# Optimization experiments

Hardware: AMD Instinct MI355X
Metric: run time of the kernel (lower is better)

The kernel has to match this reference:

```python
import jax, jax.numpy as jnp
import numpy as np

EMBED = 1024
HEADS = 16
HEAD_DIM = EMBED // HEADS
B, N = 2, 2048


def setup_inputs() -> dict:
    key = jax.random.key(0)
    ks = jax.random.split(key, 7)
    s = 1.0 / np.sqrt(EMBED)
    x = jax.random.normal(ks[0], (B, N, EMBED), dtype=jnp.float32)
    # causal mask: 1 where attention allowed, 0 elsewhere (masked_fill on mask==0)
    mask = jnp.tril(jnp.ones((N, N), dtype=jnp.int32))[None, None, :, :]
    Wq = jax.random.uniform(ks[1], (EMBED, EMBED), jnp.float32, -s, s)
    Wk = jax.random.uniform(ks[2], (EMBED, EMBED), jnp.float32, -s, s)
    Wv = jax.random.uniform(ks[3], (EMBED, EMBED), jnp.float32, -s, s)
    Wo = jax.random.uniform(ks[4], (EMBED, EMBED), jnp.float32, -s, s)
    bo = jax.random.uniform(ks[5], (EMBED,), jnp.float32, -s, s)
    return {"x": x, "mask": mask, "Wq": Wq, "Wk": Wk, "Wv": Wv, "Wo": Wo, "bo": bo}


def reference(x, mask, Wq, Wk, Wv, Wo, bo):
    Bx, Nx, D = x.shape
    # torch nn.Linear: y = x @ W.T
    q = (x @ Wq.T).reshape(Bx, Nx, HEADS, HEAD_DIM).transpose(0, 2, 1, 3)
    k = (x @ Wk.T).reshape(Bx, Nx, HEADS, HEAD_DIM).transpose(0, 2, 1, 3)
    v = (x @ Wv.T).reshape(Bx, Nx, HEADS, HEAD_DIM).transpose(0, 2, 1, 3)
    score = jnp.einsum('bhqd,bhkd->bhqk', q, k) / np.sqrt(HEAD_DIM).astype(np.float32)
    score = jnp.where(mask == 0, -jnp.inf, score)
    probs = jax.nn.softmax(score, axis=-1)
    out = jnp.einsum('bhqk,bhkd->bhqd', probs, v)  # [B,H,N,hd]
    out = out.transpose(0, 2, 1, 3).reshape(Bx, Nx, D)
    return out @ Wo.T + bo
```

## Files before the change

### kernel.cpp

```cpp
#include <hip/hip_runtime.h>
#include <hip/hip_bf16.h>

#define B_  2
#define N_  2048
#define E_  1024
#define H_  16
#define HD_ 64
#define M_  (B_*N_)
#define RSZ ((size_t)M_ * E_)

typedef short bf16x8 __attribute__((ext_vector_type(8)));
typedef float f32x4 __attribute__((ext_vector_type(4)));
typedef unsigned short u16x8 __attribute__((ext_vector_type(8)));

#define AS1 __attribute__((address_space(1)))
#define AS3 __attribute__((address_space(3)))

__device__ __forceinline__ unsigned short f2bfu(float f) {
    __hip_bfloat16 h = __float2bfloat16(f);
    return *reinterpret_cast<unsigned short*>(&h);
}
__device__ __forceinline__ unsigned int pack2bf(float lo, float hi) {
    return ((unsigned int)f2bfu(hi) << 16) | (unsigned int)f2bfu(lo);
}
#define MFMA16(a,b,c) __builtin_amdgcn_mfma_f32_16x16x32_bf16((a),(b),(c),0,0,0)

__device__ __forceinline__ void gl_lds16(const void* g, void* l) {
    __builtin_amdgcn_global_load_lds((const AS1 void*)g, (AS3 void*)l, 16, 0, 0);
}

__global__ __launch_bounds__(256) void fconv_all_kernel(
    const float* __restrict__ x,
    const float* __restrict__ Wq, const float* __restrict__ Wk,
    const float* __restrict__ Wv, const float* __restrict__ Wo,
    unsigned short* __restrict__ xbf, unsigned short* __restrict__ wbf)
{
    const int bid = blockIdx.x;
    const float* src;
    unsigned short* dst;
    int off;
    if (bid < 2048) {
        src = x; dst = xbf; off = bid * 2048 + threadIdx.x * 8;
    } else {
        const int z = (bid - 2048) >> 9;
        src = (z == 0) ? Wq : (z == 1 ? Wk : (z == 2 ? Wv : Wo));
        dst = wbf + (size_t)z * E_ * E_;
        off = ((bid - 2048) & 511) * 2048 + threadIdx.x * 8;
    }
    const float4 a = *reinterpret_cast<const float4*>(src + off);
    const float4 b = *reinterpret_cast<const float4*>(src + off + 4);
    u16x8 v;
    v[0]=f2bfu(a.x); v[1]=f2bfu(a.y); v[2]=f2bfu(a.z); v[3]=f2bfu(a.w);
    v[4]=f2bfu(b.x); v[5]=f2bfu(b.y); v[6]=f2bfu(b.z); v[7]=f2bfu(b.w);
    *reinterpret_cast<u16x8*>(dst + off) = v;
}

__global__ __launch_bounds__(256) void fconv_kernel(
    const float* __restrict__ src, unsigned short* __restrict__ dst)
{
    const int i0 = (blockIdx.x * 256 + threadIdx.x) * 8;
    const float4 a = *reinterpret_cast<const float4*>(src + i0);
    const float4 b = *reinterpret_cast<const float4*>(src + i0 + 4);
    u16x8 v;
    v[0]=f2bfu(a.x); v[1]=f2bfu(a.y); v[2]=f2bfu(a.z); v[3]=f2bfu(a.w);
    v[4]=f2bfu(b.x); v[5]=f2bfu(b.y); v[6]=f2bfu(b.z); v[7]=f2bfu(b.w);
    *reinterpret_cast<u16x8*>(dst + i0) = v;
}

__global__ __launch_bounds__(256) void qkv_glds_kernel(
    const unsigned short* __restrict__ xbf, const unsigned short* __restrict__ wbf,
    unsigned short* __restrict__ qkv)
{
    const int z = blockIdx.z;
    const unsigned short* __restrict__ W = wbf + (size_t)z * E_ * E_;
    unsigned short* __restrict__ out = qkv + (size_t)z * RSZ;
    const int m0 = blockIdx.x * 64;
    const int n0 = blockIdx.y * 128;
    __shared__ unsigned short ldsA[64*64];
    __shared__ unsigned short ldsB[128*64];
    const int t = threadIdx.x;
    const int lane = t & 63;
    const int w = t >> 6, wr = w >> 1, wc = w & 1;
    const int fr = lane & 15, fq = lane >> 4;
    const int subrow = lane >> 3;
    const int csw = ((lane & 7) ^ subrow) * 8;
    const int rcol = ((fq * 8) ^ ((fr & 7) * 8));
    f32x4 acc[2][4] = {};

    for (int kt = 0; kt < 16; ++kt) {
        const int k0 = kt * 64;
        __syncthreads();
        #pragma unroll
        for (int i = 0; i < 6; ++i) {
            const int c = w * 6 + i;
            if (c < 8) {
                const int row = c * 8 + subrow;
                gl_lds16(xbf + (size_t)(m0 + row) * E_ + k0 + csw, &ldsA[c * 512]);
            } else {
                const int row = (c - 8) * 8 + subrow;
                gl_lds16(W + (size_t)(n0 + row) * E_ + k0 + csw, &ldsB[(c - 8) * 512]);
            }
        }
        __syncthreads();
        #pragma unroll
        for (int ks = 0; ks < 2; ++ks) {
            bf16x8 af[2], bfv[4];
            #pragma unroll
            for (int mf = 0; mf < 2; ++mf)
                af[mf] = *(const bf16x8*)&ldsA[(wr*32 + mf*16 + fr)*64 + (rcol ^ (ks*32))];
            #pragma unroll
            for (int nf = 0; nf < 4; ++nf)
                bfv[nf] = *(const bf16x8*)&ldsB[(wc*64 + nf*16 + fr)*64 + (rcol ^ (ks*32))];
            #pragma unroll
            for (int mf = 0; mf < 2; ++mf)
                #pragma unroll
                for (int nf = 0; nf < 4; ++nf)
                    acc[mf][nf] = MFMA16(af[mf], bfv[nf], acc[mf][nf]);
        }
    }

    const float scale = (z == 0) ? 0.125f : 1.0f;
    #pragma unroll
    for (int mf = 0; mf < 2; ++mf) {
        #pragma unroll
        for (int r = 0; r < 4; ++r) {
            const int m = m0 + wr*32 + mf*16 + fq*4 + r;
            const int b = m >> 11, npos = m & (N_ - 1);
            #pragma unroll
            for (int nf = 0; nf < 4; ++nf) {
                const int n = n0 + wc*64 + nf*16 + fr;
                const int h = n >> 6, d = n & 63;
                const unsigned short val = f2bfu(acc[mf][nf][r] * scale);
                if (z == 2)
                    out[(((size_t)(b*H_ + h))*HD_ + d)*N_ + npos] = val;
                else
                    out[(((size_t)(b*H_ + h))*N_ + npos)*HD_ + d] = val;
            }
        }
    }
}

__global__ __launch_bounds__(256) void qkv_f32_kernel(
    const float* __restrict__ x, const unsigned short* __restrict__ wbf,
    unsigned short* __restrict__ qkv)
{
    const int z = blockIdx.z;
    const unsigned short* __restrict__ W = wbf + (size_t)z * E_ * E_;
    unsigned short* __restrict__ out = qkv + (size_t)z * RSZ;
    const int m0 = blockIdx.x * 128;
    const int n0 = blockIdx.y * 128;
    __shared__ unsigned short As[128][72];
    __shared__ unsigned short Bs[128][72];
    const int t = threadIdx.x;
    const int lane = t & 63;
    const int w = t >> 6, wr = w >> 1, wc = w & 1;
    const int fr = lane & 15, fq = lane >> 4;
    const int srow = t >> 1, scol = (t & 1) * 32;
    f32x4 acc[4][4] = {};

    const float* arow = x + (size_t)(m0 + srow) * E_ + scol;
    const unsigned short* brow = W + (size_t)(n0 + srow) * E_ + scol;

    float4 a4[8];
    u16x8 b8[4];
    #pragma unroll
    for (int i = 0; i < 8; ++i) a4[i] = reinterpret_cast<const float4*>(arow)[i];
    #pragma unroll
    for (int i = 0; i < 4; ++i) b8[i] = reinterpret_cast<const u16x8*>(brow)[i];

    for (int k0 = 0; k0 < E_; k0 += 64) {
        __syncthreads();
        #pragma unroll
        for (int j = 0; j < 4; ++j) {
            u16x8 va;
            va[0]=f2bfu(a4[2*j].x); va[1]=f2bfu(a4[2*j].y); va[2]=f2bfu(a4[2*j].z); va[3]=f2bfu(a4[2*j].w);
            va[4]=f2bfu(a4[2*j+1].x); va[5]=f2bfu(a4[2*j+1].y); va[6]=f2bfu(a4[2*j+1].z); va[7]=f2bfu(a4[2*j+1].w);
            *reinterpret_cast<u16x8*>(&As[srow][scol + 8*j]) = va;
            *reinterpret_cast<u16x8*>(&Bs[srow][scol + 8*j]) = b8[j];
        }
        __syncthreads();
        if (k0 + 64 < E_) {
            #pragma unroll
            for (int i = 0; i < 8; ++i)
                a4[i] = reinterpret_cast<const float4*>(arow + k0 + 64)[i];
            #pragma unroll
            for (int i = 0; i < 4; ++i)
                b8[i] = reinterpret_cast<const u16x8*>(brow + k0 + 64)[i];
        }
        #pragma unroll
        for (int ks = 0; ks < 2; ++ks) {
            bf16x8 af[4], bfv[4];
            #pragma unroll
            for (int mf = 0; mf < 4; ++mf)
                af[mf] = *reinterpret_cast<const bf16x8*>(&As[wr*64 + mf*16 + fr][ks*32 + fq*8]);
            #pragma unroll
            for (int nf = 0; nf < 4; ++nf)
                bfv[nf] = *reinterpret_cast<const bf16x8*>(&Bs[wc*64 + nf*16 + fr][ks*32 + fq*8]);
            #pragma unroll
            for (int mf = 0; mf < 4; ++mf)
                #pragma unroll
                for (int nf = 0; nf < 4; ++nf)
                    acc[mf][nf] = MFMA16(af[mf], bfv[nf], acc[mf][nf]);
        }
    }

    const float scale = (z == 0) ? 0.125f : 1.0f;
    #pragma unroll
    for (int mf = 0; mf < 4; ++mf) {
        #pragma unroll
        for (int r = 0; r < 4; ++r) {
            const int m = m0 + wr*64 + mf*16 + fq*4 + r;
            const int b = m >> 11, npos = m & (N_ - 1);
            #pragma unroll
            for (int nf = 0; nf < 4; ++nf) {
                const int n = n0 + wc*64 + nf*16 + fr;
                const int h = n >> 6, d = n & 63;
                const unsigned short val = f2bfu(acc[mf][nf][r] * scale);
                if (z == 2)
                    out[(((size_t)(b*H_ + h))*HD_ + d)*N_ + npos] = val;
                else
                    out[(((size_t)(b*H_ + h))*N_ + npos)*HD_ + d] = val;
            }
        }
    }
}

__global__ __launch_bounds__(512) void attn_mfma_kernel(
    const unsigned short* __restrict__ qkv, unsigned short* __restrict__ attn_out)
{
    const int bh = blockIdx.x;
    const int xp = blockIdx.y;
    const unsigned short* Qp  = qkv + (size_t)bh * N_ * HD_;
    const unsigned short* Kp  = qkv + RSZ + (size_t)bh * N_ * HD_;
    const unsigned short* Vtp = qkv + 2*RSZ + (size_t)bh * N_ * HD_;
    __shared__ unsigned short Ks[64][72], Vt[64][72];
    const int t = threadIdx.x;
    const int lane = t & 63, w = t >> 6;
    const int fr = lane & 15, fq = lane >> 4;
    const int srow = t >> 3, sc0 = (t & 7) * 8;
    const int qbase = (w < 4) ? ((31 - xp) * 64 + w * 16)
                              : (xp * 64 + (w - 4) * 16);
    const int KT = 32 - xp;
    const int ql = qbase + fr;
    const int lane_b0 = (2 * (fq & 1)) * 16 + fr;
    const int lane_b1 = lane_b0 + 16;
    const bool hi_sel = (fq >> 1) != 0;

    bf16x8 qfr[2];
    #pragma unroll
    for (int ks = 0; ks < 2; ++ks)
        qfr[ks] = *reinterpret_cast<const bf16x8*>(
            Qp + (size_t)ql * HD_ + ks*32 + fq*8);

    float m_run = -1e30f, l_run = 0.f;
    f32x4 o[4] = {};

    u16x8 kreg = *reinterpret_cast<const u16x8*>(Kp + (size_t)srow * HD_ + sc0);
    u16x8 vreg = *reinterpret_cast<const u16x8*>(Vtp + (size_t)srow * N_ + sc0);

    for (int kt = 0; kt < KT; ++kt) {
        const int k0 = kt * 64;
        __syncthreads();
        *reinterpret_cast<u16x8*>(&Ks[srow][sc0]) = kreg;
        *reinterpret_cast<u16x8*>(&Vt[srow][sc0]) = vreg;
        __syncthreads();
        if (kt + 1 < KT) {
            kreg = *reinterpret_cast<const u16x8*>(Kp + (size_t)(k0 + 64 + srow) * HD_ + sc0);
            vreg = *reinterpret_cast<const u16x8*>(Vtp + (size_t)srow * N_ + k0 + 64 + sc0);
        }
        if (k0 > qbase + 15) continue;

        f32x4 s[4] = {};
        __builtin_amdgcn_s_setprio(1);
        #pragma unroll
        for (int ks = 0; ks < 2; ++ks) {
            bf16x8 bk[4];
            #pragma unroll
            for (int nf = 0; nf < 4; ++nf)
                bk[nf] = *reinterpret_cast<const bf16x8*>(&Ks[nf*16 + fr][ks*32 + fq*8]);
            #pragma unroll
            for (int nf = 0; nf < 4; ++nf)
                s[nf] = MFMA16(bk[nf], qfr[ks], s[nf]);
        }
        __builtin_amdgcn_s_setprio(0);

        if (k0 + 63 > qbase) {
            #pragma unroll
            for (int nf = 0; nf < 4; ++nf)
                #pragma unroll
                for (int r = 0; r < 4; ++r)
                    if (k0 + nf*16 + fq*4 + r > ql) s[nf][r] = -1e30f;
        }

        float pm = -1e30f;
        #pragma unroll
        for (int nf = 0; nf < 4; ++nf)
            pm = fmaxf(pm, fmaxf(fmaxf(s[nf][0], s[nf][1]),
                                 fmaxf(s[nf][2], s[nf][3])));
        pm = fmaxf(pm, __shfl_xor(pm, 16));
        pm = fmaxf(pm, __shfl_xor(pm, 32));

        const bool need = __any(pm > m_run + 8.f);
        float scl = 1.f;
        if (need) {
            const float mnew = fmaxf(m_run, pm);
            scl = __expf(m_run - mnew);
            m_run = mnew;
        }

        float rs = 0.f;
        unsigned int u[4][2];
        #pragma unroll
        for (int nf = 0; nf < 4; ++nf) {
            const float p0 = __expf(s[nf][0] - m_run);
            const float p1 = __expf(s[nf][1] - m_run);
            const float p2 = __expf(s[nf][2] - m_run);
            const float p3 = __expf(s[nf][3] - m_run);
            rs += (p0 + p1) + (p2 + p3);
            u[nf][0] = pack2bf(p0, p1);
            u[nf][1] = pack2bf(p2, p3);
        }
        {
            float v = rs;
            v += __shfl_xor(v, 16);
            v += __shfl_xor(v, 32);
            l_run = l_run * scl + v;
        }
        if (need) {
            #pragma unroll
            for (int df = 0; df < 4; ++df)
                #pragma unroll
                for (int r = 0; r < 4; ++r)
                    o[df][r] *= scl;
        }

        bf16x8 pb[2];
        #pragma unroll
        for (int ks = 0; ks < 2; ++ks) {
            const unsigned int t00 = __shfl(u[2*ks+0][0], lane_b0);
            const unsigned int t01 = __shfl(u[2*ks+0][1], lane_b0);
            const unsigned int t02 = __shfl(u[2*ks+0][0], lane_b1);
            const unsigned int t03 = __shfl(u[2*ks+0][1], lane_b1);
            const unsigned int t10 = __shfl(u[2*ks+1][0], lane_b0);
            const unsigned int t11 = __shfl(u[2*ks+1][1], lane_b0);
            const unsigned int t12 = __shfl(u[2*ks+1][0], lane_b1);
            const unsigned int t13 = __shfl(u[2*ks+1][1], lane_b1);
            union { unsigned int wd[4]; bf16x8 v; } pu;
            pu.wd[0] = hi_sel ? t10 : t00;
            pu.wd[1] = hi_sel ? t11 : t01;
            pu.wd[2] = hi_sel ? t12 : t02;
            pu.wd[3] = hi_sel ? t13 : t03;
            pb[ks] = pu.v;
        }

        __builtin_amdgcn_s_setprio(1);
        #pragma unroll
        for (int ks = 0; ks < 2; ++ks) {
            bf16x8 bv[4];
            #pragma unroll
            for (int df = 0; df < 4; ++df)
                bv[df] = *reinterpret_cast<const bf16x8*>(&Vt[df*16 + fr][ks*32 + fq*8]);
            #pragma unroll
            for (int df = 0; df < 4; ++df)
                o[df] = MFMA16(bv[df], pb[ks], o[df]);
        }
        __builtin_amdgcn_s_setprio(0);
    }

    const int b = bh >> 4, h = bh & 15;
    const float inv = 1.0f / l_run;
    #pragma unroll
    for (int df = 0; df < 4; ++df)
        #pragma unroll
        for (int r = 0; r < 4; ++r) {
            const int d = df*16 + fq*4 + r;
            attn_out[((size_t)(b*N_ + ql))*E_ + h*64 + d] = f2bfu(o[df][r] * inv);
        }
}

__global__ __launch_bounds__(256) void out_glds_kernel(
    const unsigned short* __restrict__ A, const unsigned short* __restrict__ Wobf,
    const float* __restrict__ bo, float* __restrict__ out)
{
    const int m0 = blockIdx.x * 64;
    const int n0 = blockIdx.y * 128;
    __shared__ unsigned short ldsA[64*64];
    __shared__ unsigned short ldsB[128*64];
    const int t = threadIdx.x;
    const int lane = t & 63;
    const int w = t >> 6, wr = w >> 1, wc = w & 1;
    const int fr = lane & 15, fq = lane >> 4;
    const int subrow = lane >> 3;
    const int csw = ((lane & 7) ^ subrow) * 8;
    const int rcol = ((fq * 8) ^ ((fr & 7) * 8));
    f32x4 acc[2][4] = {};

    for (int kt = 0; kt < 16; ++kt) {
        const int k0 = kt * 64;
        __syncthreads();
        #pragma unroll
        for (int i = 0; i < 6; ++i) {
            const int c = w * 6 + i;
            if (c < 8) {
                const int row = c * 8 + subrow;
                gl_lds16(A + (size_t)(m0 + row) * E_ + k0 + csw, &ldsA[c * 512]);
            } else {
                const int row = (c - 8) * 8 + subrow;
                gl_lds16(Wobf + (size_t)(n0 + row) * E_ + k0 + csw, &ldsB[(c - 8) * 512]);
            }
        }
        __syncthreads();
        #pragma unroll
        for (int ks = 0; ks < 2; ++ks) {
            bf16x8 af[2], bfv[4];
            #pragma unroll
            for (int mf = 0; mf < 2; ++mf)
                af[mf] = *(const bf16x8*)&ldsA[(wr*32 + mf*16 + fr)*64 + (rcol ^ (ks*32))];
            #pragma unroll
            for (int nf = 0; nf < 4; ++nf)
                bfv[nf] = *(const bf16x8*)&ldsB[(wc*64 + nf*16 + fr)*64 + (rcol ^ (ks*32))];
            #pragma unroll
            for (int mf = 0; mf < 2; ++mf)
                #pragma unroll
                for (int nf = 0; nf < 4; ++nf)
                    acc[mf][nf] = MFMA16(af[mf], bfv[nf], acc[mf][nf]);
        }
    }

    #pragma unroll
    for (int mf = 0; mf < 2; ++mf) {
        #pragma unroll
        for (int r = 0; r < 4; ++r) {
            const int m = m0 + wr*32 + mf*16 + fq*4 + r;
            #pragma unroll
            for (int nf = 0; nf < 4; ++nf) {
                const int n = n0 + wc*64 + nf*16 + fr;
                out[(size_t)m * E_ + n] = acc[mf][nf][r] + bo[n];
            }
        }
    }
}

extern "C" void kernel_launch(void* const* d_in, const int* in_sizes, int n_in,
                              void* d_out, int out_size, void* d_ws, size_t ws_size,
                              hipStream_t stream) {
    const float* x  = (const float*)d_in[0];
    const float* Wq = (const float*)d_in[2];
    const float* Wk = (const float*)d_in[3];
    const float* Wv = (const float*)d_in[4];
    const float* Wo = (const float*)d_in[5];
    const float* bo = (const float*)d_in[6];
    float* out = (float*)d_out;

    unsigned short* ws = (unsigned short*)d_ws;
    const size_t need_main = 5 * RSZ * sizeof(unsigned short);

    if (ws_size >= need_main) {
        unsigned short* xbf  = ws;
        unsigned short* wbf  = ws + RSZ;
        unsigned short* qkvq = ws + 2 * RSZ;
        unsigned short* attn_ws = ws;
        unsigned short* wobf = wbf + 3 * (size_t)E_ * E_;

        fconv_all_kernel<<<4096, 256, 0, stream>>>(x, Wq, Wk, Wv, Wo, xbf, wbf);

        dim3 g1(M_ / 64, E_ / 128, 3);
        qkv_glds_kernel<<<g1, 256, 0, stream>>>(xbf, wbf, qkvq);

        dim3 g2(B_ * H_, 16);
        attn_mfma_kernel<<<g2, 512, 0, stream>>>(qkvq, attn_ws);

        dim3 g3(M_ / 64, E_ / 128);
        out_glds_kernel<<<g3, 256, 0, stream>>>(attn_ws, wobf, bo, out);
    } else {
        unsigned short* wbf = ws;
        unsigned short* qkvq = ws + RSZ;
        unsigned short* attn_ws = ws;
        unsigned short* wobf = ws + RSZ;

        const int cgrid = E_ * E_ / (256 * 8);
        fconv_kernel<<<cgrid, 256, 0, stream>>>(Wq, wbf);
        fconv_kernel<<<cgrid, 256, 0, stream>>>(Wk, wbf + (size_t)E_ * E_);
        fconv_kernel<<<cgrid, 256, 0, stream>>>(Wv, wbf + 2 * (size_t)E_ * E_);

        dim3 g1(M_ / 128, E_ / 128, 3);
        qkv_f32_kernel<<<g1, 256, 0, stream>>>(x, wbf, qkvq);

        dim3 g2(B_ * H_, 16);
        attn_mfma_kernel<<<g2, 512, 0, stream>>>(qkvq, attn_ws);

        fconv_kernel<<<cgrid, 256, 0, stream>>>(Wo, wobf);

        dim3 g3(M_ / 64, E_ / 128);
        out_glds_kernel<<<g3, 256, 0, stream>>>(attn_ws, wobf, bo, out);
    }
}
```

Baseline: 121.0 us.

## Fuse QKV projections into one GEMM pass and widen attention KV tile

The QKV projection now computes Q, K and V in a single block, sharing each loaded x tile across all three weight matrices instead of launching three z-slices that each reload x. The attention kernel processes 128 keys per iteration instead of 64, halving the iteration count and its barriers. It also uses a packed bf16 conversion instruction for the probabilities. In exchange, register pressure (three accumulator sets) and LDS use rise, the fused grid has a third as many blocks, and the wider attention tile does more masked work on diagonal tiles.

```diff
diff --git a/kernel.cpp b/kernel.cpp
--- a/kernel.cpp
+++ b/kernel.cpp
@@ -20,8 +20,10 @@
     __hip_bfloat16 h = __float2bfloat16(f);
     return *reinterpret_cast<unsigned short*>(&h);
 }
-__device__ __forceinline__ unsigned int pack2bf(float lo, float hi) {
-    return ((unsigned int)f2bfu(hi) << 16) | (unsigned int)f2bfu(lo);
+__device__ __forceinline__ unsigned int cvtpk(float lo, float hi) {
+    unsigned int r;
+    asm("v_cvt_pk_bf16_f32 %0, %1, %2" : "=v"(r) : "v"(lo), "v"(hi));
+    return r;
 }
 #define MFMA16(a,b,c) __builtin_amdgcn_mfma_f32_16x16x32_bf16((a),(b),(c),0,0,0)
 
@@ -67,17 +69,14 @@
     *reinterpret_cast<u16x8*>(dst + i0) = v;
 }
 
-__global__ __launch_bounds__(256) void qkv_glds_kernel(
+__global__ __launch_bounds__(256) void qkv_fused_kernel(
     const unsigned short* __restrict__ xbf, const unsigned short* __restrict__ wbf,
     unsigned short* __restrict__ qkv)
 {
-    const int z = blockIdx.z;
-    const unsigned short* __restrict__ W = wbf + (size_t)z * E_ * E_;
-    unsigned short* __restrict__ out = qkv + (size_t)z * RSZ;
     const int m0 = blockIdx.x * 64;
     const int n0 = blockIdx.y * 128;
     __shared__ unsigned short ldsA[64*64];
-    __shared__ unsigned short ldsB[128*64];
+    __shared__ unsigned short ldsB[3][128*64];
     const int t = threadIdx.x;
     const int lane = t & 63;
     const int w = t >> 6, wr = w >> 1, wc = w & 1;
@@ -85,56 +84,67 @@
     const int subrow = lane >> 3;
     const int csw = ((lane & 7) ^ subrow) * 8;
     const int rcol = ((fq * 8) ^ ((fr & 7) * 8));
-    f32x4 acc[2][4] = {};
+    f32x4 acc[3][2][4] = {};
 
     for (int kt = 0; kt < 16; ++kt) {
         const int k0 = kt * 64;
         __syncthreads();
         #pragma unroll
-        for (int i = 0; i < 6; ++i) {
-            const int c = w * 6 + i;
+        for (int i = 0; i < 14; ++i) {
+            const int c = w * 14 + i;
             if (c < 8) {
                 const int row = c * 8 + subrow;
                 gl_lds16(xbf + (size_t)(m0 + row) * E_ + k0 + csw, &ldsA[c * 512]);
             } else {
-                const int row = (c - 8) * 8 + subrow;
-                gl_lds16(W + (size_t)(n0 + row) * E_ + k0 + csw, &ldsB[(c - 8) * 512]);
+                const int cc = c - 8;
+                const int zb = cc >> 4, bc = cc & 15;
+                const int row = bc * 8 + subrow;
+                gl_lds16(wbf + (size_t)zb * E_ * E_ + (size_t)(n0 + row) * E_ + k0 + csw,
+                         &ldsB[zb][bc * 512]);
             }
         }
         __syncthreads();
         #pragma unroll
         for (int ks = 0; ks < 2; ++ks) {
-            bf16x8 af[2], bfv[4];
+            bf16x8 af[2];
             #pragma unroll
             for (int mf = 0; mf < 2; ++mf)
                 af[mf] = *(const bf16x8*)&ldsA[(wr*32 + mf*16 + fr)*64 + (rcol ^ (ks*32))];
             #pragma unroll
-            for (int nf = 0; nf < 4; ++nf)
-                bfv[nf] = *(const bf16x8*)&ldsB[(wc*64 + nf*16 + fr)*64 + (rcol ^ (ks*32))];
-            #pragma unroll
-            for (int mf = 0; mf < 2; ++mf)
+            for (int zb = 0; zb < 3; ++zb) {
+                bf16x8 bfv[4];
                 #pragma unroll
                 for (int nf = 0; nf < 4; ++nf)
-                    acc[mf][nf] = MFMA16(af[mf], bfv[nf], acc[mf][nf]);
-        }
-    }
-
-    const float scale = (z == 0) ? 0.125f : 1.0f;
-    #pragma unroll
-    for (int mf = 0; mf < 2; ++mf) {
-        #pragma unroll
-        for (int r = 0; r < 4; ++r) {
-            const int m = m0 + wr*32 + mf*16 + fq*4 + r;
-            const int b = m >> 11, npos = m & (N_ - 1);
-            #pragma unroll
-            for (int nf = 0; nf < 4; ++nf) {
-                const int n = n0 + wc*64 + nf*16 + fr;
-                const int h = n >> 6, d = n & 63;
-                const unsigned short val = f2bfu(acc[mf][nf][r] * scale);
-                if (z == 2)
-                    out[(((size_t)(b*H_ + h))*HD_ + d)*N_ + npos] = val;
-                else
-                    out[(((size_t)(b*H_ + h))*N_ + npos)*HD_ + d] = val;
+                    bfv[nf] = *(const bf16x8*)&ldsB[zb][(wc*64 + nf*16 + fr)*64 + (rcol ^ (ks*32))];
+                #pragma unroll
+                for (int mf = 0; mf < 2; ++mf)
+                    #pragma unroll
+                    for (int nf = 0; nf < 4; ++nf)
+                        acc[zb][mf][nf] = MFMA16(af[mf], bfv[nf], acc[zb][mf][nf]);
+            }
+        }
+    }
+
+    #pragma unroll
+    for (int zb = 0; zb < 3; ++zb) {
+        unsigned short* __restrict__ out = qkv + (size_t)zb * RSZ;
+        const float scale = (zb == 0) ? 0.125f : 1.0f;
+        #pragma unroll
+        for (int mf = 0; mf < 2; ++mf) {
+            #pragma unroll
+            for (int r = 0; r < 4; ++r) {
+                const int m = m0 + wr*32 + mf*16 + fq*4 + r;
+                const int b = m >> 11, npos = m & (N_ - 1);
+                #pragma unroll
+                for (int nf = 0; nf < 4; ++nf) {
+                    const int n = n0 + wc*64 + nf*16 + fr;
+                    const int h = n >> 6, d = n & 63;
+                    const unsigned short val = f2bfu(acc[zb][mf][nf][r] * scale);
+                    if (zb == 2)
+                        out[(((size_t)(b*H_ + h))*HD_ + d)*N_ + npos] = val;
+                    else
+                        out[(((size_t)(b*H_ + h))*N_ + npos)*HD_ + d] = val;
+                }
             }
         }
     }
@@ -233,14 +243,15 @@
     const unsigned short* Qp  = qkv + (size_t)bh * N_ * HD_;
     const unsigned short* Kp  = qkv + RSZ + (size_t)bh * N_ * HD_;
     const unsigned short* Vtp = qkv + 2*RSZ + (size_t)bh * N_ * HD_;
-    __shared__ unsigned short Ks[64][72], Vt[64][72];
+    __shared__ unsigned short Ks[128][72], Vt[64][136];
     const int t = threadIdx.x;
     const int lane = t & 63, w = t >> 6;
     const int fr = lane & 15, fq = lane >> 4;
-    const int srow = t >> 3, sc0 = (t & 7) * 8;
+    const int srK = t >> 2, scK = (t & 3) * 16;
+    const int srV = t >> 3, scV = (t & 7) * 16;
     const int qbase = (w < 4) ? ((31 - xp) * 64 + w * 16)
                               : (xp * 64 + (w - 4) * 16);
-    const int KT = 32 - xp;
+    const int KT = (33 - xp) >> 1;
     const int ql = qbase + fr;
     const int lane_b0 = (2 * (fq & 1)) * 16 + fr;
     const int lane_b1 = lane_b0 + 16;
@@ -255,38 +266,43 @@
     float m_run = -1e30f, l_run = 0.f;
     f32x4 o[4] = {};
 
-    u16x8 kreg = *reinterpret_cast<const u16x8*>(Kp + (size_t)srow * HD_ + sc0);
-    u16x8 vreg = *reinterpret_cast<const u16x8*>(Vtp + (size_t)srow * N_ + sc0);
+    u16x8 kra = *reinterpret_cast<const u16x8*>(Kp + (size_t)srK * HD_ + scK);
+    u16x8 krb = *reinterpret_cast<const u16x8*>(Kp + (size_t)srK * HD_ + scK + 8);
+    u16x8 vra = *reinterpret_cast<const u16x8*>(Vtp + (size_t)srV * N_ + scV);
+    u16x8 vrb = *reinterpret_cast<const u16x8*>(Vtp + (size_t)srV * N_ + scV + 8);
 
     for (int kt = 0; kt < KT; ++kt) {
-        const int k0 = kt * 64;
-        __syncthreads();
-        *reinterpret_cast<u16x8*>(&Ks[srow][sc0]) = kreg;
-        *reinterpret_cast<u16x8*>(&Vt[srow][sc0]) = vreg;
+        const int k0 = kt * 128;
+        __syncthreads();
+        *reinterpret_cast<u16x8*>(&Ks[srK][scK])     = kra;
+        *reinterpret_cast<u16x8*>(&Ks[srK][scK + 8]) = krb;
+        *reinterpret_cast<u16x8*>(&Vt[srV][scV])     = vra;
+        *reinterpret_cast<u16x8*>(&Vt[srV][scV + 8]) = vrb;
         __syncthreads();
         if (kt + 1 < KT) {
-            kreg = *reinterpret_cast<const u16x8*>(Kp + (size_t)(k0 + 64 + srow) * HD_ + sc0);
-            vreg = *reinterpret_cast<const u16x8*>(Vtp + (size_t)srow * N_ + k0 + 64 + sc0);
+            const int kn = k0 + 128;
+            kra = *reinterpret_cast<const u16x8*>(Kp + (size_t)(kn + srK) * HD_ + scK);
+            krb = *reinterpret_cast<const u16x8*>(Kp + (size_t)(kn + srK) * HD_ + scK + 8);
+            vra = *reinterpret_cast<const u16x8*>(Vtp + (size_t)srV * N_ + kn + scV);
+            vrb = *reinterpret_cast<const u16x8*>(Vtp + (size_t)srV * N_ + kn + scV + 8);
         }
         if (k0 > qbase + 15) continue;
 
-        f32x4 s[4] = {};
+        f32x4 s[8] = {};
         __builtin_amdgcn_s_setprio(1);
         #pragma unroll
         for (int ks = 0; ks < 2; ++ks) {
-            bf16x8 bk[4];
-            #pragma unroll
-            for (int nf = 0; nf < 4; ++nf)
-                bk[nf] = *reinterpret_cast<const bf16x8*>(&Ks[nf*16 + fr][ks*32 + fq*8]);
-            #pragma unroll
-            for (int nf = 0; nf < 4; ++nf)
-                s[nf] = MFMA16(bk[nf], qfr[ks], s[nf]);
+            #pragma unroll
+            for (int nf = 0; nf < 8; ++nf) {
+                bf16x8 bk = *reinterpret_cast<const bf16x8*>(&Ks[nf*16 + fr][ks*32 + fq*8]);
+                s[nf] = MFMA16(bk, qfr[ks], s[nf]);
+            }
         }
         __builtin_amdgcn_s_setprio(0);
 
-        if (k0 + 63 > qbase) {
-            #pragma unroll
-            for (int nf = 0; nf < 4; ++nf)
+        if (k0 + 127 > qbase) {
+            #pragma unroll
+            for (int nf = 0; nf < 8; ++nf)
                 #pragma unroll
                 for (int r = 0; r < 4; ++r)
                     if (k0 + nf*16 + fq*4 + r > ql) s[nf][r] = -1e30f;
@@ -294,7 +310,7 @@
 
         float pm = -1e30f;
         #pragma unroll
-        for (int nf = 0; nf < 4; ++nf)
+        for (int nf = 0; nf < 8; ++nf)
             pm = fmaxf(pm, fmaxf(fmaxf(s[nf][0], s[nf][1]),
                                  fmaxf(s[nf][2], s[nf][3])));
         pm = fmaxf(pm, __shfl_xor(pm, 16));
@@ -309,16 +325,16 @@
         }
 
         float rs = 0.f;
-        unsigned int u[4][2];
-        #pragma unroll
-        for (int nf = 0; nf < 4; ++nf) {
+        unsigned int u[8][2];
+        #pragma unroll
+        for (int nf = 0; nf < 8; ++nf) {
             const float p0 = __expf(s[nf][0] - m_run);
             const float p1 = __expf(s[nf][1] - m_run);
             const float p2 = __expf(s[nf][2] - m_run);
             const float p3 = __expf(s[nf][3] - m_run);
             rs += (p0 + p1) + (p2 + p3);
-            u[nf][0] = pack2bf(p0, p1);
-            u[nf][1] = pack2bf(p2, p3);
+            u[nf][0] = cvtpk(p0, p1);
+            u[nf][1] = cvtpk(p2, p3);
         }
         {
             float v = rs;
@@ -334,35 +350,35 @@
                     o[df][r] *= scl;
         }
 
-        bf16x8 pb[2];
-        #pragma unroll
-        for (int ks = 0; ks < 2; ++ks) {
-            const unsigned int t00 = __shfl(u[2*ks+0][0], lane_b0);
-            const unsigned int t01 = __shfl(u[2*ks+0][1], lane_b0);
-            const unsigned int t02 = __shfl(u[2*ks+0][0], lane_b1);
-            const unsigned int t03 = __shfl(u[2*ks+0][1], lane_b1);
-            const unsigned int t10 = __shfl(u[2*ks+1][0], lane_b0);
-            const unsigned int t11 = __shfl(u[2*ks+1][1], lane_b0);
-            const unsigned int t12 = __shfl(u[2*ks+1][0], lane_b1);
-            const unsigned int t13 = __shfl(u[2*ks+1][1], lane_b1);
+        bf16x8 pb[4];
+        #pragma unroll
+        for (int kk = 0; kk < 4; ++kk) {
+            const unsigned int t00 = __shfl(u[2*kk+0][0], lane_b0);
+            const unsigned int t01 = __shfl(u[2*kk+0][1], lane_b0);
+            const unsigned int t02 = __shfl(u[2*kk+0][0], lane_b1);
+            const unsigned int t03 = __shfl(u[2*kk+0][1], lane_b1);
+            const unsigned int t10 = __shfl(u[2*kk+1][0], lane_b0);
+            const unsigned int t11 = __shfl(u[2*kk+1][1], lane_b0);
+            const unsigned int t12 = __shfl(u[2*kk+1][0], lane_b1);
+            const unsigned int t13 = __shfl(u[2*kk+1][1], lane_b1);
             union { unsigned int wd[4]; bf16x8 v; } pu;
             pu.wd[0] = hi_sel ? t10 : t00;
             pu.wd[1] = hi_sel ? t11 : t01;
             pu.wd[2] = hi_sel ? t12 : t02;
             pu.wd[3] = hi_sel ? t13 : t03;
-            pb[ks] = pu.v;
+            pb[kk] = pu.v;
         }
 
         __builtin_amdgcn_s_setprio(1);
         #pragma unroll
-        for (int ks = 0; ks < 2; ++ks) {
+        for (int kk = 0; kk < 4; ++kk) {
             bf16x8 bv[4];
             #pragma unroll
             for (int df = 0; df < 4; ++df)
-                bv[df] = *reinterpret_cast<const bf16x8*>(&Vt[df*16 + fr][ks*32 + fq*8]);
+                bv[df] = *reinterpret_cast<const bf16x8*>(&Vt[df*16 + fr][kk*32 + fq*8]);
             #pragma unroll
             for (int df = 0; df < 4; ++df)
-                o[df] = MFMA16(bv[df], pb[ks], o[df]);
+                o[df] = MFMA16(bv[df], pb[kk], o[df]);
         }
         __builtin_amdgcn_s_setprio(0);
     }
@@ -464,8 +480,8 @@
 
         fconv_all_kernel<<<4096, 256, 0, stream>>>(x, Wq, Wk, Wv, Wo, xbf, wbf);
 
-        dim3 g1(M_ / 64, E_ / 128, 3);
-        qkv_glds_kernel<<<g1, 256, 0, stream>>>(xbf, wbf, qkvq);
+        dim3 g1(M_ / 64, E_ / 128);
+        qkv_fused_kernel<<<g1, 256, 0, stream>>>(xbf, wbf, qkvq);
 
         dim3 g2(B_ * H_, 16);
         attn_mfma_kernel<<<g2, 512, 0, stream>>>(qkvq, attn_ws);
```

Measured after the change: 105.9 us. -12.5%, faster.
